# Kernel tuning notes

Measured on AMD Instinct MI355X. Metric: run time of the kernel, lower is better.

## Reference

```python
import jax, jax.numpy as jnp
import numpy as np

N = 100000   # nodes
E = 1600000  # edges
G = 512      # graphs
IN_F = 128
HID = 64
EPS = 1e-5


def setup_inputs() -> dict:
    key = jax.random.key(0)
    ks = jax.random.split(key, 16)
    x = jax.random.normal(ks[0], (N, IN_F), dtype=jnp.float32)
    edge_index = jax.random.randint(ks[1], (2, E), 0, N, dtype=jnp.int64)
    batch = jnp.sort(jax.random.randint(ks[2], (N,), 0, G, dtype=jnp.int64))
    s = 0.05
    return {
        'x': x, 'edge_index': edge_index, 'batch': batch,
        'W1': jax.random.normal(ks[3], (IN_F, HID), jnp.float32) * s,
        'b1': jax.random.normal(ks[4], (HID,), jnp.float32) * s,
        'g1': jax.random.uniform(ks[5], (HID,), jnp.float32),
        'be1': jax.random.normal(ks[6], (HID,), jnp.float32) * s,
        'rm1': jnp.zeros((HID,), jnp.float32),
        'rv1': jnp.ones((HID,), jnp.float32),
        'W2': jax.random.normal(ks[7], (HID, HID), jnp.float32) * s,
        'b2': jax.random.normal(ks[8], (HID,), jnp.float32) * s,
        'g2': jax.random.uniform(ks[9], (HID,), jnp.float32),
        'be2': jax.random.normal(ks[10], (HID,), jnp.float32) * s,
        'rm2': jnp.zeros((HID,), jnp.float32),
        'rv2': jnp.ones((HID,), jnp.float32),
        'Wh1': jax.random.normal(ks[11], (2 * HID, HID), jnp.float32) * s,
        'bh1': jax.random.normal(ks[12], (HID,), jnp.float32) * s,
        'Wh2': jax.random.normal(ks[13], (HID, HID // 2), jnp.float32) * s,
        'bh2': jnp.zeros((HID // 2,), jnp.float32),
        'Wh3': jax.random.normal(ks[14], (HID // 2, 1), jnp.float32) * s,
        'bh3': jnp.zeros((1,), jnp.float32),
    }


def _gcn(h, W, b, src, dst):
    # GCNConv with added self-loops and symmetric D^{-1/2} A D^{-1/2} normalization
    hw = h @ W                                   # [N, HID]
    deg = jnp.ones((N,), hw.dtype).at[dst].add(1.0)  # in-degree + self-loop
    dinv = jax.lax.rsqrt(deg)
    norm = dinv[src] * dinv[dst]                 # [E]
    agg = jax.ops.segment_sum(hw[src] * norm[:, None], dst, num_segments=N)
    return agg + hw * (dinv * dinv)[:, None] + b  # self-loop term + bias


def _bn(x, g, b, rm, rv):
    return (x - rm) * jax.lax.rsqrt(rv + EPS) * g + b


def reference(x, edge_index, batch, W1, b1, g1, be1, rm1, rv1,
              W2, b2, g2, be2, rm2, rv2, Wh1, bh1, Wh2, bh2, Wh3, bh3):
    src, dst = edge_index[0], edge_index[1]
    # layer 0 (no residual: dim change 128 -> 64)
    h = jax.nn.relu(_bn(_gcn(x, W1, b1, src, dst), g1, be1, rm1, rv1))
    # layer 1 with residual
    h = h + jax.nn.relu(_bn(_gcn(h, W2, b2, src, dst), g2, be2, rm2, rv2))
    # global mean + max pooling per graph
    ones = jnp.ones((N,), h.dtype)
    cnt = jnp.maximum(jax.ops.segment_sum(ones, batch, num_segments=G), 1.0)
    h_mean = jax.ops.segment_sum(h, batch, num_segments=G) / cnt[:, None]
    h_max = jax.ops.segment_max(h, batch, num_segments=G)
    hg = jnp.concatenate([h_mean, h_max], axis=-1)   # [G, 2*HID]
    # MLP head (dropout disabled in eval)
    z = jax.nn.relu(hg @ Wh1 + bh1)
    z = jax.nn.relu(z @ Wh2 + bh2)
    out = z @ Wh3 + bh3
    return jax.nn.sigmoid(out).squeeze(-1)           # [G]
```

## Files before the change

### kernel.cpp

```cpp
#include <hip/hip_runtime.h>
#include <math.h>

#define NN 100000
#define EE 1600000
#define GG 512
#define INF_ 128
#define HID 64
#define EPS 1e-5f

#define NBUK 391
#define P1_TILES 98
#define GB_B 25
#define GEMM1_B 1563

typedef unsigned int uint32;
typedef __attribute__((ext_vector_type(8))) short bf16x8;
typedef __attribute__((ext_vector_type(4))) float f32x4;
typedef __attribute__((ext_vector_type(2))) float f32x2;

static __device__ inline uint32 f2bf(float f) {
    uint32 u = __float_as_uint(f);
    return (u + 0x7FFFu + ((u >> 16) & 1u)) >> 16;
}


template <int K, bool SCALE>
__device__ __forceinline__ void gemm_body(const float* __restrict__ X,
        const float* __restrict__ W, const float* __restrict__ dinv,
        uint32* __restrict__ outb, int nrows, int bx,
        unsigned short* __restrict__ Al, unsigned short* __restrict__ Bl) {
    constexpr int KP = K + 8;
    int tid = threadIdx.x;
    for (int i = tid; i < 64 * (K / 2); i += 256) {
        int n = i & 63, kp = i >> 6;
        uint32 lo = f2bf(W[(size_t)(2 * kp) * 64 + n]);
        uint32 hi = f2bf(W[(size_t)(2 * kp + 1) * 64 + n]);
        *(uint32*)&Bl[n * KP + kp * 2] = lo | (hi << 16);
    }
    int r0 = bx * 64;
    const float* Xb = X + (size_t)r0 * K;
    int limit = (nrows - r0) * K;
    for (int f = tid * 4; f < 64 * K; f += 1024) {
        float4 v = {0.f, 0.f, 0.f, 0.f};
        if (f + 3 < limit) v = *(const float4*)&Xb[f];
        int row = f / K, kpos = f % K;
        ushort4 pk;
        pk.x = (unsigned short)f2bf(v.x);
        pk.y = (unsigned short)f2bf(v.y);
        pk.z = (unsigned short)f2bf(v.z);
        pk.w = (unsigned short)f2bf(v.w);
        *(ushort4*)&Al[row * KP + kpos] = pk;
    }
    __syncthreads();
    int lane = tid & 63, wv = tid >> 6;
    int m = lane & 15, quad = lane >> 4;
    f32x4 acc0 = {0.f, 0.f, 0.f, 0.f}, acc1 = acc0, acc2 = acc0, acc3 = acc0;
    int arow = wv * 16 + m;
#pragma unroll
    for (int k0 = 0; k0 < K; k0 += 32) {
        int koff = k0 + quad * 8;
        bf16x8 a = *(const bf16x8*)&Al[arow * KP + koff];
        bf16x8 b0 = *(const bf16x8*)&Bl[(0 * 16 + m) * KP + koff];
        bf16x8 b1 = *(const bf16x8*)&Bl[(1 * 16 + m) * KP + koff];
        bf16x8 b2 = *(const bf16x8*)&Bl[(2 * 16 + m) * KP + koff];
        bf16x8 b3 = *(const bf16x8*)&Bl[(3 * 16 + m) * KP + koff];
        acc0 = __builtin_amdgcn_mfma_f32_16x16x32_bf16(a, b0, acc0, 0, 0, 0);
        acc1 = __builtin_amdgcn_mfma_f32_16x16x32_bf16(a, b1, acc1, 0, 0, 0);
        acc2 = __builtin_amdgcn_mfma_f32_16x16x32_bf16(a, b2, acc2, 0, 0, 0);
        acc3 = __builtin_amdgcn_mfma_f32_16x16x32_bf16(a, b3, acc3, 0, 0, 0);
    }
    float dv[4];
#pragma unroll
    for (int reg = 0; reg < 4; ++reg) {
        int row = r0 + wv * 16 + quad * 4 + reg;
        if (SCALE) dv[reg] = (row < nrows) ? dinv[row] : 0.f;
        else       dv[reg] = 1.f;
    }
    const float* accs[4] = {(const float*)&acc0, (const float*)&acc1,
                            (const float*)&acc2, (const float*)&acc3};
#pragma unroll
    for (int nt = 0; nt < 4; ++nt) {
#pragma unroll
        for (int reg = 0; reg < 4; ++reg) {
            float val = accs[nt][reg] * dv[reg];
            float v1 = __shfl_down(val, 1);
            float v2 = __shfl_down(val, 2);
            float v3 = __shfl_down(val, 3);
            int row = r0 + wv * 16 + quad * 4 + reg;
            if (((m & 3) == 0) && row < nrows) {
                int u = __builtin_amdgcn_cvt_pk_fp8_f32(val, v1, 0, false);
                u = __builtin_amdgcn_cvt_pk_fp8_f32(v2, v3, u, true);
                outb[(size_t)row * 16 + nt * 4 + (m >> 2)] = (uint32)u;
            }
        }
    }
}

__global__ __launch_bounds__(256) void k_mega(const int* __restrict__ ei,
        int* __restrict__ hblk, const int* __restrict__ bat, int* __restrict__ gb,
        const float* __restrict__ x, const float* __restrict__ W1,
        uint32* __restrict__ hwb) {
    __shared__ alignas(16) char smem[64 * (INF_ + 8) * 2 * 2];
    int b = blockIdx.x, t = threadIdx.x;
    if (b < P1_TILES) {
        int* h = (int*)smem;
        for (int i = t; i < NBUK; i += 256) h[i] = 0;
        __syncthreads();
        const int4* dst4 = (const int4*)(ei + EE);
        int base4 = b * 4096;
        for (int j = 0; j < 16; ++j) {
            int i4 = base4 + j * 256 + t;
            if (i4 < EE / 4) {
                int4 d = dst4[i4];
                atomicAdd(&h[d.x >> 8], 1);
                atomicAdd(&h[d.y >> 8], 1);
                atomicAdd(&h[d.z >> 8], 1);
                atomicAdd(&h[d.w >> 8], 1);
            }
        }
        __syncthreads();
        for (int i = t; i < NBUK; i += 256) hblk[b * NBUK + i] = h[i];
    } else if (b < P1_TILES + GB_B) {
        int gid = (b - P1_TILES) * 256 + t;
        for (int i = gid; i < NN; i += GB_B * 256) {
            int bi = bat[i];
            if (i == 0) {
                for (int g = 0; g <= bi; ++g) gb[g] = 0;
            } else {
                int bp = bat[i - 1];
                for (int g = bp + 1; g <= bi; ++g) gb[g] = i;
            }
            if (i == NN - 1)
                for (int g = bi + 1; g <= GG; ++g) gb[g] = NN;
        }
    } else {
        int bx = b - P1_TILES - GB_B;
        unsigned short* Al = (unsigned short*)smem;
        unsigned short* Bl = (unsigned short*)(smem + 64 * (INF_ + 8) * 2);
        gemm_body<INF_, false>(x, W1, nullptr, hwb, NN, bx, Al, Bl);
    }
}

__global__ void k_scan2(const int* __restrict__ hblk, int* __restrict__ bbase,
                        int* __restrict__ rbase, int* __restrict__ offs,
                        uint32* __restrict__ hwb,
                        const float* b1, const float* g1, const float* be1,
                        const float* rm1, const float* rv1,
                        const float* b2, const float* g2, const float* be2,
                        const float* rm2, const float* rv2, float* sc) {
    __shared__ int wsum[8];
    int t = threadIdx.x;
    int lane = t & 63, w = t >> 6;
    if (t < 16) hwb[(size_t)NN * 16 + t] = 0u;
    if (t >= 448) {
        int l = t - 448;
        float s1 = g1[l] * rsqrtf(rv1[l] + EPS);
        sc[l]       = s1;
        sc[64 + l]  = (b1[l] - rm1[l]) * s1 + be1[l];
        float s2 = g2[l] * rsqrtf(rv2[l] + EPS);
        sc[128 + l] = s2;
        sc[192 + l] = (b2[l] - rm2[l]) * s2 + be2[l];
    }
    int c = 0;
    if (t < NBUK)
        for (int b = 0; b < P1_TILES; ++b) c += hblk[b * NBUK + t];
    int v = c;
    for (int d = 1; d < 64; d <<= 1) { int n = __shfl_up(v, d); if (lane >= d) v += n; }
    if (lane == 63) wsum[w] = v;
    __syncthreads();
    int pre = 0;
    for (int q = 0; q < w; ++q) pre += wsum[q];
    int excl = pre + v - c;
    if (t <= NBUK) bbase[t] = excl;
    if (t == 0) offs[NN] = EE;
    if (t < NBUK) {
        int run = excl;
        for (int b = 0; b < P1_TILES; ++b) {
            rbase[b * NBUK + t] = run;
            run += hblk[b * NBUK + t];
        }
    }
}

__global__ __launch_bounds__(256) void k_p1b(const int* __restrict__ ei,
                                             const int* __restrict__ rbase,
                                             uint32* __restrict__ pairs) {
    __shared__ int h[NBUK];
    int b = blockIdx.x, t = threadIdx.x;
    for (int i = t; i < NBUK; i += 256) h[i] = rbase[b * NBUK + i];
    __syncthreads();
    const int4* src4 = (const int4*)ei;
    const int4* dst4 = (const int4*)(ei + EE);
    int base4 = b * 4096;
    for (int j = 0; j < 16; ++j) {
        int i4 = base4 + j * 256 + t;
        if (i4 < EE / 4) {
            int4 d = dst4[i4];
            int4 s = src4[i4];
            int p0 = atomicAdd(&h[d.x >> 8], 1);
            pairs[p0] = ((uint32)s.x << 8) | (uint32)(d.x & 255);
            int p1 = atomicAdd(&h[d.y >> 8], 1);
            pairs[p1] = ((uint32)s.y << 8) | (uint32)(d.y & 255);
            int p2 = atomicAdd(&h[d.z >> 8], 1);
            pairs[p2] = ((uint32)s.z << 8) | (uint32)(d.z & 255);
            int p3 = atomicAdd(&h[d.w >> 8], 1);
            pairs[p3] = ((uint32)s.w << 8) | (uint32)(d.w & 255);
        }
    }
}

__global__ __launch_bounds__(256) void k_p2(const uint32* __restrict__ pairs,
                                            const int* __restrict__ bbase,
                                            int* __restrict__ offs, float* __restrict__ dinv,
                                            int* __restrict__ col) {
    int b = blockIdx.x, t = threadIdx.x;
    int nbase = b << 8;
    int ebase = bbase[b], eend = bbase[b + 1];
    int m = eend - ebase;
    __shared__ int cnt[256];
    __shared__ int wsum[4];
    cnt[t] = 0;
    __syncthreads();
    for (int i = t; i < m; i += 256)
        atomicAdd(&cnt[pairs[ebase + i] & 255u], 1);
    __syncthreads();
    int c = cnt[t];
    int lane = t & 63, w = t >> 6;
    int v = c;
    for (int d = 1; d < 64; d <<= 1) { int n = __shfl_up(v, d); if (lane >= d) v += n; }
    if (lane == 63) wsum[w] = v;
    __syncthreads();
    int pre = 0;
    for (int q = 0; q < w; ++q) pre += wsum[q];
    int excl = pre + v - c;
    int node = nbase + t;
    if (node < NN) {
        offs[node] = ebase + excl;
        dinv[node] = rsqrtf(1.f + (float)c);
    }
    __syncthreads();
    cnt[t] = excl;
    __syncthreads();
    for (int i = t; i < m; i += 256) {
        uint32 u = pairs[ebase + i];
        int loc = atomicAdd(&cnt[u & 255u], 1);
        col[ebase + loc] = (int)(u >> 8);
    }
}

__global__ void k_gcn_gather_w(const uint32* __restrict__ hwb, const int* __restrict__ col,
                               const int* __restrict__ offs,
                               const float* __restrict__ dinv, const float* __restrict__ scale,
                               const float* __restrict__ shift,
                               float* __restrict__ out) {
    int node = blockIdx.x * 4 + (threadIdx.x >> 6);
    if (node >= NN) return;
    int lane = threadIdx.x & 63;
    int quarter = lane >> 4;
    int fl = lane & 15;
    int e0 = offs[node], e1 = offs[node + 1];
    float di = dinv[node];
    uint32 uself = hwb[(size_t)node * 16 + fl];
    float a0 = 0.f, a1 = 0.f, a2 = 0.f, a3 = 0.f;
    float b0 = 0.f, b1 = 0.f, b2 = 0.f, b3 = 0.f;
    for (int base = e0; base < e1; base += 64) {
        int m = e1 - base; if (m > 64) m = 64;
        int srcv = NN; float wv = 0.f;
        if (lane < m) { srcv = col[base + lane]; wv = dinv[srcv]; }
        for (int j = 0; j < m; j += 16) {
            int   s0 = __shfl(srcv, j + quarter);
            int   s1 = __shfl(srcv, j + 4 + quarter);
            int   s2 = __shfl(srcv, j + 8 + quarter);
            int   s3 = __shfl(srcv, j + 12 + quarter);
            float w0 = __shfl(wv, j + quarter);
            float w1 = __shfl(wv, j + 4 + quarter);
            float w2 = __shfl(wv, j + 8 + quarter);
            float w3 = __shfl(wv, j + 12 + quarter);
            uint32 u0 = hwb[(size_t)s0 * 16 + fl];
            uint32 u1 = hwb[(size_t)s1 * 16 + fl];
            uint32 u2 = hwb[(size_t)s2 * 16 + fl];
            uint32 u3 = hwb[(size_t)s3 * 16 + fl];
            f32x2 l0 = __builtin_amdgcn_cvt_pk_f32_fp8((int)u0, false);
            f32x2 h0 = __builtin_amdgcn_cvt_pk_f32_fp8((int)u0, true);
            f32x2 l1 = __builtin_amdgcn_cvt_pk_f32_fp8((int)u1, false);
            f32x2 h1 = __builtin_amdgcn_cvt_pk_f32_fp8((int)u1, true);
            f32x2 l2 = __builtin_amdgcn_cvt_pk_f32_fp8((int)u2, false);
            f32x2 h2 = __builtin_amdgcn_cvt_pk_f32_fp8((int)u2, true);
            f32x2 l3 = __builtin_amdgcn_cvt_pk_f32_fp8((int)u3, false);
            f32x2 h3 = __builtin_amdgcn_cvt_pk_f32_fp8((int)u3, true);
            a0 = fmaf(l0[0], w0, a0); a1 = fmaf(l0[1], w0, a1);
            a2 = fmaf(h0[0], w0, a2); a3 = fmaf(h0[1], w0, a3);
            b0 = fmaf(l1[0], w1, b0); b1 = fmaf(l1[1], w1, b1);
            b2 = fmaf(h1[0], w1, b2); b3 = fmaf(h1[1], w1, b3);
            a0 = fmaf(l2[0], w2, a0); a1 = fmaf(l2[1], w2, a1);
            a2 = fmaf(h2[0], w2, a2); a3 = fmaf(h2[1], w2, a3);
            b0 = fmaf(l3[0], w3, b0); b1 = fmaf(l3[1], w3, b1);
            b2 = fmaf(h3[0], w3, b2); b3 = fmaf(h3[1], w3, b3);
        }
    }
    a0 += b0; a1 += b1; a2 += b2; a3 += b3;
    a0 += __shfl_xor(a0, 16); a0 += __shfl_xor(a0, 32);
    a1 += __shfl_xor(a1, 16); a1 += __shfl_xor(a1, 32);
    a2 += __shfl_xor(a2, 16); a2 += __shfl_xor(a2, 32);
    a3 += __shfl_xor(a3, 16); a3 += __shfl_xor(a3, 32);
    if (quarter == 0) {
        f32x2 slo = __builtin_amdgcn_cvt_pk_f32_fp8((int)uself, false);
        f32x2 shi = __builtin_amdgcn_cvt_pk_f32_fp8((int)uself, true);
        float dii = di * di;
        float4 sc4 = *(const float4*)&scale[4 * fl];
        float4 sh4 = *(const float4*)&shift[4 * fl];
        float v0 = fmaf(a0 * di + slo[0] * dii, sc4.x, sh4.x);
        float v1 = fmaf(a1 * di + slo[1] * dii, sc4.y, sh4.y);
        float v2 = fmaf(a2 * di + shi[0] * dii, sc4.z, sh4.z);
        float v3 = fmaf(a3 * di + shi[1] * dii, sc4.w, sh4.w);
        float4 o;
        o.x = fmaxf(v0, 0.f); o.y = fmaxf(v1, 0.f);
        o.z = fmaxf(v2, 0.f); o.w = fmaxf(v3, 0.f);
        *(float4*)&out[(size_t)node * 64 + 4 * fl] = o;
    }
}

__global__ void k_gcn_gather(const uint32* __restrict__ hwb, const int* __restrict__ col,
                             const int* __restrict__ offs,
                             const float* __restrict__ dinv, const float* __restrict__ scale,
                             const float* __restrict__ shift, const float* __restrict__ resid,
                             float* __restrict__ out) {
    int node = blockIdx.x * 4 + (threadIdx.x >> 6);
    if (node >= NN) return;
    int lane = threadIdx.x & 63;
    int quarter = lane >> 4;
    int fl = lane & 15;
    int e0 = offs[node], e1 = offs[node + 1];
    float di = dinv[node];
    uint32 uself = hwb[(size_t)node * 16 + fl];
    float a0 = 0.f, a1 = 0.f, a2 = 0.f, a3 = 0.f;
    float b0 = 0.f, b1 = 0.f, b2 = 0.f, b3 = 0.f;
    for (int base = e0; base < e1; base += 64) {
        int m = e1 - base; if (m > 64) m = 64;
        int srcv = NN;
        if (lane < m) srcv = col[base + lane];
        for (int j = 0; j < m; j += 16) {
            int s0 = __shfl(srcv, j + quarter);
            int s1 = __shfl(srcv, j + 4 + quarter);
            int s2 = __shfl(srcv, j + 8 + quarter);
            int s3 = __shfl(srcv, j + 12 + quarter);
            uint32 u0 = hwb[(size_t)s0 * 16 + fl];
            uint32 u1 = hwb[(size_t)s1 * 16 + fl];
            uint32 u2 = hwb[(size_t)s2 * 16 + fl];
            uint32 u3 = hwb[(size_t)s3 * 16 + fl];
            f32x2 l0 = __builtin_amdgcn_cvt_pk_f32_fp8((int)u0, false);
            f32x2 h0 = __builtin_amdgcn_cvt_pk_f32_fp8((int)u0, true);
            f32x2 l1 = __builtin_amdgcn_cvt_pk_f32_fp8((int)u1, false);
            f32x2 h1 = __builtin_amdgcn_cvt_pk_f32_fp8((int)u1, true);
            f32x2 l2 = __builtin_amdgcn_cvt_pk_f32_fp8((int)u2, false);
            f32x2 h2 = __builtin_amdgcn_cvt_pk_f32_fp8((int)u2, true);
            f32x2 l3 = __builtin_amdgcn_cvt_pk_f32_fp8((int)u3, false);
            f32x2 h3 = __builtin_amdgcn_cvt_pk_f32_fp8((int)u3, true);
            a0 += l0[0]; a1 += l0[1]; a2 += h0[0]; a3 += h0[1];
            b0 += l1[0]; b1 += l1[1]; b2 += h1[0]; b3 += h1[1];
            a0 += l2[0]; a1 += l2[1]; a2 += h2[0]; a3 += h2[1];
            b0 += l3[0]; b1 += l3[1]; b2 += h3[0]; b3 += h3[1];
        }
    }
    a0 += b0; a1 += b1; a2 += b2; a3 += b3;
    a0 += __shfl_xor(a0, 16); a0 += __shfl_xor(a0, 32);
    a1 += __shfl_xor(a1, 16); a1 += __shfl_xor(a1, 32);
    a2 += __shfl_xor(a2, 16); a2 += __shfl_xor(a2, 32);
    a3 += __shfl_xor(a3, 16); a3 += __shfl_xor(a3, 32);
    if (quarter == 0) {
        f32x2 slo = __builtin_amdgcn_cvt_pk_f32_fp8((int)uself, false);
        f32x2 shi = __builtin_amdgcn_cvt_pk_f32_fp8((int)uself, true);
        float4 sc4 = *(const float4*)&scale[4 * fl];
        float4 sh4 = *(const float4*)&shift[4 * fl];
        float v0 = fmaf((a0 + slo[0]) * di, sc4.x, sh4.x);
        float v1 = fmaf((a1 + slo[1]) * di, sc4.y, sh4.y);
        float v2 = fmaf((a2 + shi[0]) * di, sc4.z, sh4.z);
        float v3 = fmaf((a3 + shi[1]) * di, sc4.w, sh4.w);
        float4 rv = *(const float4*)&resid[(size_t)node * 64 + 4 * fl];
        float4 o;
        o.x = fmaxf(v0, 0.f) + rv.x;
        o.y = fmaxf(v1, 0.f) + rv.y;
        o.z = fmaxf(v2, 0.f) + rv.z;
        o.w = fmaxf(v3, 0.f) + rv.w;
        *(float4*)&out[(size_t)node * 64 + 4 * fl] = o;
    }
}

__global__ void k_poolhead(const float* __restrict__ h, const int* __restrict__ gb,
                           const float* __restrict__ Wh1, const float* __restrict__ bh1,
                           const float* __restrict__ Wh2, const float* __restrict__ bh2,
                           const float* __restrict__ Wh3, const float* __restrict__ bh3,
                           float* __restrict__ out) {
    int g = blockIdx.x, t = threadIdx.x;
    int lo = gb[g], hi = gb[g + 1];
    float s0 = 0.f, s1 = 0.f, s2 = 0.f, s3 = 0.f;
    float s4 = 0.f, s5 = 0.f, s6 = 0.f, s7 = 0.f;
    float m0 = 0.f, m1 = 0.f, m2 = 0.f, m3 = 0.f;
    float m4 = 0.f, m5 = 0.f, m6 = 0.f, m7 = 0.f;
    int i = lo;
    for (; i + 8 <= hi; i += 8) {
        float v0 = h[(size_t)(i + 0) * 64 + t];
        float v1 = h[(size_t)(i + 1) * 64 + t];
        float v2 = h[(size_t)(i + 2) * 64 + t];
        float v3 = h[(size_t)(i + 3) * 64 + t];
        float v4 = h[(size_t)(i + 4) * 64 + t];
        float v5 = h[(size_t)(i + 5) * 64 + t];
        float v6 = h[(size_t)(i + 6) * 64 + t];
        float v7 = h[(size_t)(i + 7) * 64 + t];
        s0 += v0; m0 = fmaxf(m0, v0);
        s1 += v1; m1 = fmaxf(m1, v1);
        s2 += v2; m2 = fmaxf(m2, v2);
        s3 += v3; m3 = fmaxf(m3, v3);
        s4 += v4; m4 = fmaxf(m4, v4);
        s5 += v5; m5 = fmaxf(m5, v5);
        s6 += v6; m6 = fmaxf(m6, v6);
        s7 += v7; m7 = fmaxf(m7, v7);
    }
    for (; i < hi; ++i) {
        float v = h[(size_t)i * 64 + t];
        s0 += v; m0 = fmaxf(m0, v);
    }
    float sum = ((s0 + s1) + (s2 + s3)) + ((s4 + s5) + (s6 + s7));
    float mx = fmaxf(fmaxf(fmaxf(m0, m1), fmaxf(m2, m3)),
                     fmaxf(fmaxf(m4, m5), fmaxf(m6, m7)));
    float c = fmaxf((float)(hi - lo), 1.f);
    __shared__ float hg[128];
    __shared__ float z1[64];
    __shared__ float z2[32];
    hg[t]      = sum / c;
    hg[64 + t] = mx;
    __syncthreads();
    float acc = bh1[t];
#pragma unroll 8
    for (int k = 0; k < 128; ++k) acc = fmaf(hg[k], Wh1[k * 64 + t], acc);
    z1[t] = fmaxf(acc, 0.f);
    __syncthreads();
    if (t < 32) {
        float a2 = bh2[t];
#pragma unroll 8
        for (int k = 0; k < 64; ++k) a2 = fmaf(z1[k], Wh2[k * 32 + t], a2);
        z2[t] = fmaxf(a2, 0.f);
    }
    __syncthreads();
    if (t == 0) {
        float a3 = bh3[0];
        for (int k = 0; k < 32; ++k) a3 = fmaf(z2[k], Wh3[k], a3);
        out[g] = 1.f / (1.f + expf(-a3));
    }
}

__global__ __launch_bounds__(256) void k_gemm2(const float* __restrict__ X,
                                               const float* __restrict__ W,
                                               const float* __restrict__ dinv,
                                               uint32* __restrict__ outb) {
    __shared__ alignas(16) unsigned short Al[64 * (HID + 8)];
    __shared__ alignas(16) unsigned short Bl[64 * (HID + 8)];
    gemm_body<HID, true>(X, W, dinv, outb, NN, blockIdx.x, Al, Bl);
}


static inline size_t alignup(size_t x) { return (x + 255) & ~(size_t)255; }

extern "C" void kernel_launch(void* const* d_in, const int* in_sizes, int n_in,
                              void* d_out, int out_size, void* d_ws, size_t ws_size,
                              hipStream_t stream) {
    const float* x   = (const float*)d_in[0];
    const int*   ei  = (const int*)d_in[1];
    const int*   bat = (const int*)d_in[2];
    const float* W1  = (const float*)d_in[3];
    const float* b1  = (const float*)d_in[4];
    const float* g1  = (const float*)d_in[5];
    const float* be1 = (const float*)d_in[6];
    const float* rm1 = (const float*)d_in[7];
    const float* rv1 = (const float*)d_in[8];
    const float* W2  = (const float*)d_in[9];
    const float* b2  = (const float*)d_in[10];
    const float* g2  = (const float*)d_in[11];
    const float* be2 = (const float*)d_in[12];
    const float* rm2 = (const float*)d_in[13];
    const float* rv2 = (const float*)d_in[14];
    const float* Wh1 = (const float*)d_in[15];
    const float* bh1 = (const float*)d_in[16];
    const float* Wh2 = (const float*)d_in[17];
    const float* bh2 = (const float*)d_in[18];
    const float* Wh3 = (const float*)d_in[19];
    const float* bh3 = (const float*)d_in[20];
    float* out = (float*)d_out;

    char* ws = (char*)d_ws;
    size_t o = 0;
    int*   hblk   = (int*)(ws + o);  o = alignup(o + (size_t)P1_TILES * NBUK * 4);
    int*   rbase  = (int*)(ws + o);  o = alignup(o + (size_t)P1_TILES * NBUK * 4);
    int*   bbase  = (int*)(ws + o);  o = alignup(o + (NBUK + 1) * 4);
    int*   offs   = (int*)(ws + o);  o = alignup(o + (NN + 1) * 4);
    uint32* pairs = (uint32*)(ws + o); o = alignup(o + (size_t)EE * 4);
    int*   col    = (int*)(ws + o);  o = alignup(o + (size_t)EE * 4);
    float* dinv   = (float*)(ws + o); o = alignup(o + (size_t)NN * 4);
    float* scb    = (float*)(ws + o); o = alignup(o + 4 * 64 * 4);
    int*   gb     = (int*)(ws + o);  o = alignup(o + (GG + 1) * 4);
    uint32* hwb   = (uint32*)(ws + o); o = alignup(o + (size_t)(NN + 1) * 16 * 4);
    float* h      = (float*)(ws + o); o = alignup(o + (size_t)NN * 64 * 4);
    (void)ws_size; (void)n_in; (void)in_sizes; (void)out_size;

    k_mega<<<P1_TILES + GB_B + GEMM1_B, 256, 0, stream>>>(ei, hblk, bat, gb,
                                                          x, W1, hwb);
    k_scan2<<<1, 512, 0, stream>>>(hblk, bbase, rbase, offs, hwb,
                                   b1, g1, be1, rm1, rv1, b2, g2, be2, rm2, rv2, scb);
    k_p1b<<<P1_TILES, 256, 0, stream>>>(ei, rbase, pairs);
    k_p2<<<NBUK, 256, 0, stream>>>(pairs, bbase, offs, dinv, col);

    k_gcn_gather_w<<<(NN + 3) / 4, 256, 0, stream>>>(hwb, col, offs, dinv,
                                                     scb, scb + 64, h);
    k_gemm2<<<GEMM1_B, 256, 0, stream>>>(h, W2, dinv, hwb);
    k_gcn_gather<<<(NN + 3) / 4, 256, 0, stream>>>(hwb, col, offs, dinv,
                                                   scb + 128, scb + 192, h, h);
    k_poolhead<<<GG, 64, 0, stream>>>(h, gb, Wh1, bh1, Wh2, bh2, Wh3, bh3, out);
}
```

Measured before the change: 285.9 us.

## Fuse single-block scan into scatter kernel with transposed per-tile histogram layout

Measured after the change: 284.8 us. About the same (-0.4%).

```diff
diff --git a/kernel.cpp b/kernel.cpp
--- a/kernel.cpp
+++ b/kernel.cpp
@@ -10,6 +10,7 @@
 
 #define NBUK 391
 #define P1_TILES 98
+#define P1_PAD 104
 #define GB_B 25
 #define GEMM1_B 1563
 
@@ -99,7 +100,11 @@
 __global__ __launch_bounds__(256) void k_mega(const int* __restrict__ ei,
         int* __restrict__ hblk, const int* __restrict__ bat, int* __restrict__ gb,
         const float* __restrict__ x, const float* __restrict__ W1,
-        uint32* __restrict__ hwb) {
+        uint32* __restrict__ hwb,
+        const float* b1, const float* g1, const float* be1,
+        const float* rm1, const float* rv1,
+        const float* b2, const float* g2, const float* be2,
+        const float* rm2, const float* rv2, float* sc) {
     __shared__ alignas(16) char smem[64 * (INF_ + 8) * 2 * 2];
     int b = blockIdx.x, t = threadIdx.x;
     if (b < P1_TILES) {
@@ -119,7 +124,7 @@
             }
         }
         __syncthreads();
-        for (int i = t; i < NBUK; i += 256) hblk[b * NBUK + i] = h[i];
+        for (int i = t; i < NBUK; i += 256) hblk[i * P1_PAD + b] = h[i];
     } else if (b < P1_TILES + GB_B) {
         int gid = (b - P1_TILES) * 256 + t;
         for (int i = gid; i < NN; i += GB_B * 256) {
@@ -133,37 +138,51 @@
             if (i == NN - 1)
                 for (int g = bi + 1; g <= GG; ++g) gb[g] = NN;
         }
+    } else if (b < P1_TILES + GB_B + 1) {
+        if (t < 64) {
+            int l = t;
+            float s1 = g1[l] * rsqrtf(rv1[l] + EPS);
+            sc[l]       = s1;
+            sc[64 + l]  = (b1[l] - rm1[l]) * s1 + be1[l];
+            float s2 = g2[l] * rsqrtf(rv2[l] + EPS);
+            sc[128 + l] = s2;
+            sc[192 + l] = (b2[l] - rm2[l]) * s2 + be2[l];
+        } else if (t < 80) {
+            hwb[(size_t)NN * 16 + (t - 64)] = 0u;
+        }
+        for (int i = t; i < NBUK * (P1_PAD - P1_TILES); i += 256) {
+            int k = i / (P1_PAD - P1_TILES);
+            int bb = P1_TILES + i % (P1_PAD - P1_TILES);
+            hblk[k * P1_PAD + bb] = 0;
+        }
     } else {
-        int bx = b - P1_TILES - GB_B;
+        int bx = b - P1_TILES - GB_B - 1;
         unsigned short* Al = (unsigned short*)smem;
         unsigned short* Bl = (unsigned short*)(smem + 64 * (INF_ + 8) * 2);
         gemm_body<INF_, false>(x, W1, nullptr, hwb, NN, bx, Al, Bl);
     }
 }
 
-__global__ void k_scan2(const int* __restrict__ hblk, int* __restrict__ bbase,
-                        int* __restrict__ rbase, int* __restrict__ offs,
-                        uint32* __restrict__ hwb,
-                        const float* b1, const float* g1, const float* be1,
-                        const float* rm1, const float* rv1,
-                        const float* b2, const float* g2, const float* be2,
-                        const float* rm2, const float* rv2, float* sc) {
+__global__ __launch_bounds__(512) void k_p1b(const int* __restrict__ ei,
+                                             const int* __restrict__ hblk,
+                                             uint32* __restrict__ pairs,
+                                             int* __restrict__ bbase,
+                                             int* __restrict__ offs) {
+    __shared__ int h[NBUK];
     __shared__ int wsum[8];
-    int t = threadIdx.x;
+    int b = blockIdx.x, t = threadIdx.x;
+    int part = 0, c = 0;
+    if (t < NBUK) {
+        const int4* row = (const int4*)(hblk + t * P1_PAD);
+#pragma unroll
+        for (int q = 0; q < P1_PAD / 4; ++q) {
+            int4 v = row[q];
+            c += v.x + v.y + v.z + v.w;
+            part += ((4 * q + 0 < b) ? v.x : 0) + ((4 * q + 1 < b) ? v.y : 0)
+                  + ((4 * q + 2 < b) ? v.z : 0) + ((4 * q + 3 < b) ? v.w : 0);
+        }
+    }
     int lane = t & 63, w = t >> 6;
-    if (t < 16) hwb[(size_t)NN * 16 + t] = 0u;
-    if (t >= 448) {
-        int l = t - 448;
-        float s1 = g1[l] * rsqrtf(rv1[l] + EPS);
-        sc[l]       = s1;
-        sc[64 + l]  = (b1[l] - rm1[l]) * s1 + be1[l];
-        float s2 = g2[l] * rsqrtf(rv2[l] + EPS);
-        sc[128 + l] = s2;
-        sc[192 + l] = (b2[l] - rm2[l]) * s2 + be2[l];
-    }
-    int c = 0;
-    if (t < NBUK)
-        for (int b = 0; b < P1_TILES; ++b) c += hblk[b * NBUK + t];
     int v = c;
     for (int d = 1; d < 64; d <<= 1) { int n = __shfl_up(v, d); if (lane >= d) v += n; }
     if (lane == 63) wsum[w] = v;
@@ -171,29 +190,17 @@
     int pre = 0;
     for (int q = 0; q < w; ++q) pre += wsum[q];
     int excl = pre + v - c;
-    if (t <= NBUK) bbase[t] = excl;
-    if (t == 0) offs[NN] = EE;
-    if (t < NBUK) {
-        int run = excl;
-        for (int b = 0; b < P1_TILES; ++b) {
-            rbase[b * NBUK + t] = run;
-            run += hblk[b * NBUK + t];
-        }
-    }
-}
-
-__global__ __launch_bounds__(256) void k_p1b(const int* __restrict__ ei,
-                                             const int* __restrict__ rbase,
-                                             uint32* __restrict__ pairs) {
-    __shared__ int h[NBUK];
-    int b = blockIdx.x, t = threadIdx.x;
-    for (int i = t; i < NBUK; i += 256) h[i] = rbase[b * NBUK + i];
+    if (t < NBUK) h[t] = excl + part;
+    if (b == 0) {
+        if (t <= NBUK) bbase[t] = excl;
+        if (t == 0) offs[NN] = EE;
+    }
     __syncthreads();
     const int4* src4 = (const int4*)ei;
     const int4* dst4 = (const int4*)(ei + EE);
     int base4 = b * 4096;
-    for (int j = 0; j < 16; ++j) {
-        int i4 = base4 + j * 256 + t;
+    for (int j = 0; j < 8; ++j) {
+        int i4 = base4 + j * 512 + t;
         if (i4 < EE / 4) {
             int4 d = dst4[i4];
             int4 s = src4[i4];
@@ -489,8 +496,7 @@
 
     char* ws = (char*)d_ws;
     size_t o = 0;
-    int*   hblk   = (int*)(ws + o);  o = alignup(o + (size_t)P1_TILES * NBUK * 4);
-    int*   rbase  = (int*)(ws + o);  o = alignup(o + (size_t)P1_TILES * NBUK * 4);
+    int*   hblk   = (int*)(ws + o);  o = alignup(o + (size_t)NBUK * P1_PAD * 4);
     int*   bbase  = (int*)(ws + o);  o = alignup(o + (NBUK + 1) * 4);
     int*   offs   = (int*)(ws + o);  o = alignup(o + (NN + 1) * 4);
     uint32* pairs = (uint32*)(ws + o); o = alignup(o + (size_t)EE * 4);
@@ -502,11 +508,10 @@
     float* h      = (float*)(ws + o); o = alignup(o + (size_t)NN * 64 * 4);
     (void)ws_size; (void)n_in; (void)in_sizes; (void)out_size;
 
-    k_mega<<<P1_TILES + GB_B + GEMM1_B, 256, 0, stream>>>(ei, hblk, bat, gb,
-                                                          x, W1, hwb);
-    k_scan2<<<1, 512, 0, stream>>>(hblk, bbase, rbase, offs, hwb,
-                                   b1, g1, be1, rm1, rv1, b2, g2, be2, rm2, rv2, scb);
-    k_p1b<<<P1_TILES, 256, 0, stream>>>(ei, rbase, pairs);
+    k_mega<<<P1_TILES + GB_B + 1 + GEMM1_B, 256, 0, stream>>>(
+        ei, hblk, bat, gb, x, W1, hwb,
+        b1, g1, be1, rm1, rv1, b2, g2, be2, rm2, rv2, scb);
+    k_p1b<<<P1_TILES, 512, 0, stream>>>(ei, hblk, pairs, bbase, offs);
     k_p2<<<NBUK, 256, 0, stream>>>(pairs, bbase, offs, dinv, col);
 
     k_gcn_gather_w<<<(NN + 3) / 4, 256, 0, stream>>>(hwb, col, offs, dinv,
```
